# Kernel tuning notes

Hardware: AMD Instinct MI355X
Metric: run time of the kernel (lower is better)

The kernel has to match this reference:

```python
import jax, jax.numpy as jnp
import numpy as np

EPS = 1e-5
N_HEADS = 8
CLAMP = 100.0


def layernorm(x, g, b):
    m = x.mean(-1, keepdims=True)
    v = x.var(-1, keepdims=True)  # biased var, matches torch LayerNorm
    return (x - m) / jnp.sqrt(v + EPS) * g + b


def depthwise7(x, w, b):
    # x: [B,C,H,W], w: [C,1,7,7] depthwise (groups=C), pad=3
    y = jax.lax.conv_general_dilated(
        x, w, window_strides=(1, 1), padding=[(3, 3), (3, 3)],
        dimension_numbers=('NCHW', 'OIHW', 'NCHW'),
        feature_group_count=x.shape[1])
    return y + b[None, :, None, None]


def setup_inputs() -> dict:
    key = jax.random.key(0)
    ks = jax.random.split(key, 12)
    B, N, C = 8, 4096, 512
    KH = 7
    s = 0.02
    return {
        'x': jax.random.normal(ks[0], (B, N, C), jnp.float32),
        'qkv_w': jax.random.normal(ks[1], (C, 3 * C), jnp.float32) * s,
        'qkv_b': jnp.zeros((3 * C,), jnp.float32),
        'out_w': jax.random.normal(ks[2], (C, C), jnp.float32) * s,
        'out_b': jnp.zeros((C,), jnp.float32),
        'pre_g': jnp.ones((C,), jnp.float32),
        'pre_b': jnp.zeros((C,), jnp.float32),
        'lcm_g': jnp.ones((C,), jnp.float32),
        'lcm_b': jnp.zeros((C,), jnp.float32),
        'ci_w': jax.random.normal(ks[3], (C, 1, KH, KH), jnp.float32) * s,
        'ci_b': jnp.zeros((C,), jnp.float32),
        'bn_g': jnp.ones((C,), jnp.float32),
        'bn_b': jnp.zeros((C,), jnp.float32),
        'co_w': jax.random.normal(ks[4], (C, 1, KH, KH), jnp.float32) * s,
        'co_b': jnp.zeros((C,), jnp.float32),
        'H': 64,
        'W': 64,
    }


def reference(x, qkv_w, qkv_b, out_w, out_b, pre_g, pre_b, lcm_g, lcm_b,
              ci_w, ci_b, bn_g, bn_b, co_w, co_b, H, W):
    B, N, C = x.shape
    hd = C // N_HEADS
    normed = layernorm(x, pre_g, pre_b)
    qkv = normed @ qkv_w + qkv_b                       # [B,N,3C]
    qkv = qkv.reshape(B, N, 3, N_HEADS, hd).transpose(2, 0, 3, 1, 4)
    q = jax.nn.relu(qkv[0])                            # [B,h,N,d]
    k = jax.nn.relu(qkv[1])
    v = qkv[2]
    kv = jnp.einsum('bhnd,bhnv->bhdv', k, v)           # O(N d^2) associativity trick
    normalizer = jnp.maximum(k.sum(2, keepdims=True), CLAMP)  # [B,h,1,d]
    attn = jnp.einsum('bhnd,bhdv->bhnv', q, kv)
    denom = jnp.maximum((q * normalizer).sum(-1, keepdims=True), CLAMP)
    attn = attn / denom
    attn = attn.transpose(0, 2, 1, 3).reshape(B, N, C)
    attn = attn @ out_w + out_b
    # Local Concentration Module on lcm_norm(attn)
    t = layernorm(attn, lcm_g, lcm_b)
    xi = t.transpose(0, 2, 1).reshape(B, C, H, W)
    y = depthwise7(xi, ci_w, ci_b)
    y = jax.nn.gelu(y, approximate=False)
    m = y.mean((0, 2, 3), keepdims=True)               # BatchNorm2d training-mode stats
    var = y.var((0, 2, 3), keepdims=True)
    y = (y - m) / jnp.sqrt(var + EPS) * bn_g[None, :, None, None] + bn_b[None, :, None, None]
    y = depthwise7(y, co_w, co_b)
    lcm_out = y.reshape(B, C, N).transpose(0, 2, 1)
    return x + attn + lcm_out
```

## Files before the change

### kernel.cpp

```cpp
#include <hip/hip_runtime.h>
#include <math.h>

typedef short v8s __attribute__((ext_vector_type(8)));
typedef short v4s __attribute__((ext_vector_type(4)));
typedef float v4f __attribute__((ext_vector_type(4)));

__device__ __forceinline__ float b2f(unsigned short u) {
    return __uint_as_float(((unsigned)u) << 16);
}
__device__ __forceinline__ unsigned short f2b(float f) {
    unsigned u = __float_as_uint(f);
    unsigned r = (u + 0x7FFF + ((u >> 16) & 1)) >> 16;
    return (unsigned short)r;
}
__device__ __forceinline__ int swz8(int row) { return (row & 7) ^ ((row >> 3) & 7); }

__device__ __forceinline__ void gl_lds16(const unsigned short* g, unsigned short* l) {
    __builtin_amdgcn_global_load_lds(
        (const __attribute__((address_space(1))) void*)g,
        (__attribute__((address_space(3))) void*)l,
        16, 0, 0);
}

__global__ __launch_bounds__(256) void zero_fill(float* __restrict__ p, int n) {
    int i = blockIdx.x * 256 + threadIdx.x;
    if (i < n) p[i] = 0.0f;
}

__global__ __launch_bounds__(256) void ln_apply(const float* __restrict__ x,
                                                const float* __restrict__ g,
                                                const float* __restrict__ bt,
                                                unsigned short* __restrict__ out) {
    int t = threadIdx.x;
    int lane = t & 63, wave = t >> 6;
    size_t row = (size_t)blockIdx.x * 4 + wave;
    const float* p = x + row * 512 + lane * 8;
    float4 va = *(const float4*)p;
    float4 vb = *(const float4*)(p + 4);
    float s = va.x + va.y + va.z + va.w + vb.x + vb.y + vb.z + vb.w;
    float s2 = va.x * va.x + va.y * va.y + va.z * va.z + va.w * va.w +
               vb.x * vb.x + vb.y * vb.y + vb.z * vb.z + vb.w * vb.w;
    for (int o = 32; o > 0; o >>= 1) {
        s += __shfl_xor(s, o);
        s2 += __shfl_xor(s2, o);
    }
    float mean = s * (1.0f / 512.0f);
    float var = s2 * (1.0f / 512.0f) - mean * mean;
    float inv = rsqrtf(var + 1e-5f);
    float4 g0 = *(const float4*)(g + lane * 8);
    float4 g1 = *(const float4*)(g + lane * 8 + 4);
    float4 b0 = *(const float4*)(bt + lane * 8);
    float4 b1 = *(const float4*)(bt + lane * 8 + 4);
    v8s o8;
    o8[0] = (short)f2b((va.x - mean) * inv * g0.x + b0.x);
    o8[1] = (short)f2b((va.y - mean) * inv * g0.y + b0.y);
    o8[2] = (short)f2b((va.z - mean) * inv * g0.z + b0.z);
    o8[3] = (short)f2b((va.w - mean) * inv * g0.w + b0.w);
    o8[4] = (short)f2b((vb.x - mean) * inv * g1.x + b1.x);
    o8[5] = (short)f2b((vb.y - mean) * inv * g1.y + b1.y);
    o8[6] = (short)f2b((vb.z - mean) * inv * g1.z + b1.z);
    o8[7] = (short)f2b((vb.w - mean) * inv * g1.w + b1.w);
    *(v8s*)&out[row * 512 + lane * 8] = o8;
}

__global__ __launch_bounds__(256) void transpose_f2b(const float* __restrict__ in,
                                                     unsigned short* __restrict__ out,
                                                     int R, int C) {
    __shared__ unsigned short tile[32][33];
    int c0 = blockIdx.x * 32, r0 = blockIdx.y * 32;
    int tx = threadIdx.x, ty = threadIdx.y;
    for (int j = 0; j < 32; j += 8)
        tile[ty + j][tx] = f2b(in[(size_t)(r0 + ty + j) * C + c0 + tx]);
    __syncthreads();
    for (int j = 0; j < 32; j += 8)
        out[(size_t)(c0 + ty + j) * R + r0 + tx] = tile[tx][ty + j];
}

template <int NB, bool QKV>
__global__ __launch_bounds__(512, 4) void gemm256(const unsigned short* __restrict__ A,
                                                  const unsigned short* __restrict__ Bt,
                                                  const float* __restrict__ bias,
                                                  unsigned short* __restrict__ o0,
                                                  unsigned short* __restrict__ o1,
                                                  unsigned short* __restrict__ o2) {
    __shared__ __align__(16) unsigned short LB[3][12288];
    int t = threadIdx.x;
    int wave = t >> 6, lane = t & 63;
    int wm = wave >> 1, wn = wave & 1;
    int mrow = lane & 15, kq4 = lane >> 4;
    int nwg = gridDim.x;
    int cpx = nwg >> 3;
    int bid = blockIdx.x;
    int swz = (bid & 7) * cpx + (bid >> 3);
    int n0 = (swz % NB) * 128;
    int m0 = (swz / NB) * 256;
    const unsigned short* Ab = A + (size_t)m0 * 512;
    const unsigned short* Bb = Bt + (size_t)n0 * 512;
    int rA0 = t >> 2;
    int cA0 = (((t & 3) ^ ((rA0 >> 1) & 3)) * 8);
    int rA1 = 128 + (t >> 2);
    int cA1 = (((t & 3) ^ ((rA1 >> 1) & 3)) * 8);
    size_t srcA0 = (size_t)rA0 * 512 + cA0;
    size_t srcA1 = (size_t)rA1 * 512 + cA1;
    unsigned offA0 = wave * 512;
    unsigned offA1 = 4096 + wave * 512;
    unsigned offB  = 8192 + wave * 512;
    v4f acc[4][4] = {};
    int swr = ((kq4 ^ ((mrow >> 1) & 3)) * 8);

#define STAGE(kt, slot)                                          \
    do {                                                         \
        const unsigned short* aS = Ab + (size_t)(kt) * 32;       \
        const unsigned short* bS = Bb + (size_t)(kt) * 32;       \
        gl_lds16(aS + srcA0, &LB[slot][offA0]);                  \
        gl_lds16(aS + srcA1, &LB[slot][offA1]);                  \
        gl_lds16(bS + srcA0, &LB[slot][offB]);                   \
    } while (0)

    STAGE(0, 0);
    STAGE(1, 1);
    asm volatile("s_waitcnt vmcnt(3)" ::: "memory");
    __builtin_amdgcn_s_barrier();
    asm volatile("" ::: "memory");
    v8s cA[4], cB[4];
    {
        const unsigned short* as = LB[0];
        const unsigned short* bs = as + 8192;
#pragma unroll
        for (int i = 0; i < 4; i++) {
            cA[i] = *(const v8s*)&as[(wm * 64 + i * 16 + mrow) * 32 + swr];
            cB[i] = *(const v8s*)&bs[(wn * 64 + i * 16 + mrow) * 32 + swr];
        }
    }
#pragma unroll
    for (int kt = 0; kt < 16; ++kt) {
        __builtin_amdgcn_s_barrier();
        asm volatile("" ::: "memory");
        if (kt + 2 < 16) STAGE(kt + 2, (kt + 2) % 3);
        __builtin_amdgcn_s_setprio(1);
#pragma unroll
        for (int i = 0; i < 2; i++)
#pragma unroll
            for (int j = 0; j < 4; j++)
                acc[i][j] = __builtin_amdgcn_mfma_f32_16x16x32_bf16(cA[i], cB[j], acc[i][j], 0, 0, 0);
        v8s nA[4], nB[4];
        if (kt < 15) {
            if (kt < 14) {
                asm volatile("s_waitcnt vmcnt(3)" ::: "memory");
            } else {
                asm volatile("s_waitcnt vmcnt(0)" ::: "memory");
            }
            __builtin_amdgcn_s_barrier();
            asm volatile("" ::: "memory");
            const unsigned short* as = LB[(kt + 1) % 3];
            const unsigned short* bs = as + 8192;
#pragma unroll
            for (int i = 0; i < 4; i++) {
                nA[i] = *(const v8s*)&as[(wm * 64 + i * 16 + mrow) * 32 + swr];
                nB[i] = *(const v8s*)&bs[(wn * 64 + i * 16 + mrow) * 32 + swr];
            }
        }
#pragma unroll
        for (int i = 2; i < 4; i++)
#pragma unroll
            for (int j = 0; j < 4; j++)
                acc[i][j] = __builtin_amdgcn_mfma_f32_16x16x32_bf16(cA[i], cB[j], acc[i][j], 0, 0, 0);
        __builtin_amdgcn_s_setprio(0);
        if (kt < 15) {
#pragma unroll
            for (int i = 0; i < 4; i++) { cA[i] = nA[i]; cB[i] = nB[i]; }
        }
    }
#undef STAGE
    __syncthreads();
    unsigned short* CT = &LB[0][0];
    bool doRelu = QKV && (n0 < 1024);
#pragma unroll
    for (int j = 0; j < 4; j++) {
        int col = wn * 64 + j * 16 + mrow;
        float bv = bias[n0 + col];
        int gr = col >> 3, gb = col & 7;
#pragma unroll
        for (int i = 0; i < 4; i++) {
            int rowb = wm * 64 + i * 16 + kq4 * 4;
#pragma unroll
            for (int r = 0; r < 4; r++) {
                int row = rowb + r;
                float v = acc[i][j][r] + bv;
                if (doRelu) v = fmaxf(v, 0.0f);
                CT[row * 136 + ((gr ^ swz8(row)) << 3) + gb] = f2b(v);
            }
        }
    }
    __syncthreads();
    if (!QKV || n0 < 512) {
#pragma unroll
        for (int p = 0; p < 8; p++) {
            int g = p * 512 + t;
            int row = g >> 4, gl = g & 15;
            v8s v = *(const v8s*)&CT[row * 136 + ((gl ^ swz8(row)) << 3)];
            *(v8s*)&o0[(size_t)(m0 + row) * 512 + n0 + gl * 8] = v;
        }
    } else {
        unsigned short* Tb = (n0 < 1024) ? o1 : o2;
        int col = t >> 2, sub = t & 3;
        int cglob = n0 + col;
        int hl = (cglob & 511) >> 6, d = cglob & 63;
        int bb = m0 >> 12, gc = m0 & 4095;
        unsigned short* dst = Tb + ((size_t)((bb * 8 + hl) * 64 + d)) * 4096 + gc;
        int cg = col >> 3, cb7 = col & 7;
#pragma unroll
        for (int g = 0; g < 8; g++) {
            v8s v;
#pragma unroll
            for (int e = 0; e < 8; e++) {
                int rr = g * 32 + sub * 8 + e;
                v[e] = (short)CT[rr * 136 + ((cg ^ swz8(rr)) << 3) + cb7];
            }
            *(v8s*)&dst[g * 32 + sub * 8] = v;
        }
    }
}

__global__ __launch_bounds__(256) void kv_part(const unsigned short* __restrict__ kT,
                                               const unsigned short* __restrict__ vT,
                                               float* __restrict__ kvp,
                                               float* __restrict__ ksp) {
    __shared__ __align__(16) unsigned short LB[3][4096];
    int bh = blockIdx.x, nc = blockIdx.y;
    int t = threadIdx.x;
    int w = t >> 6, lane = t & 63;
    int wdk = w >> 1, wdv = w & 1;
    int mrow = lane & 15, kq4 = lane >> 4;
    const unsigned short* Kb = kT + (size_t)bh * 262144 + nc * 512;
    const unsigned short* Vb = vT + (size_t)bh * 262144 + nc * 512;
    int rA = t >> 2;
    int lcA = (t & 3) ^ (rA & 3);
    size_t srcoff = (size_t)rA * 4096 + lcA * 8;
    unsigned dstK = w * 512;
    unsigned dstV = 2048 + w * 512;
    v4f acc[2][2] = {};
    v4f accs[2] = {};
    v8s ones;
#pragma unroll
    for (int jj = 0; jj < 8; jj++) ones[jj] = (short)0x3F80;

#define KSTAGE(ks, slot)                                         \
    do {                                                         \
        gl_lds16(Kb + (size_t)(ks) * 32 + srcoff, &LB[slot][dstK]); \
        gl_lds16(Vb + (size_t)(ks) * 32 + srcoff, &LB[slot][dstV]); \
    } while (0)

    KSTAGE(0, 0);
    KSTAGE(1, 1);
    for (int ks = 0; ks < 16; ++ks) {
        if (ks < 15) {
            asm volatile("s_waitcnt vmcnt(2)" ::: "memory");
        } else {
            asm volatile("s_waitcnt vmcnt(0)" ::: "memory");
        }
        __builtin_amdgcn_s_barrier();
        asm volatile("" ::: "memory");
        if (ks + 2 < 16) KSTAGE(ks + 2, (ks + 2) % 3);
        const unsigned short* as = LB[ks % 3];
        v8s af[2], bf[2];
#pragma unroll
        for (int i = 0; i < 2; i++) {
            int row = wdk * 32 + i * 16 + mrow;
            af[i] = *(const v8s*)&as[row * 32 + ((kq4 ^ (row & 3)) << 3)];
        }
#pragma unroll
        for (int j = 0; j < 2; j++) {
            int row = wdv * 32 + j * 16 + mrow;
            bf[j] = *(const v8s*)&as[2048 + row * 32 + ((kq4 ^ (row & 3)) << 3)];
        }
#pragma unroll
        for (int i = 0; i < 2; i++)
#pragma unroll
            for (int j = 0; j < 2; j++)
                acc[i][j] = __builtin_amdgcn_mfma_f32_16x16x32_bf16(af[i], bf[j], acc[i][j], 0, 0, 0);
        if (wdv == 0) {
#pragma unroll
            for (int i = 0; i < 2; i++)
                accs[i] = __builtin_amdgcn_mfma_f32_16x16x32_bf16(af[i], ones, accs[i], 0, 0, 0);
        }
    }
#undef KSTAGE
    float* dst = kvp + ((size_t)(bh * 8 + nc)) * 4096;
#pragma unroll
    for (int i = 0; i < 2; i++)
#pragma unroll
        for (int j = 0; j < 2; j++)
#pragma unroll
            for (int r = 0; r < 4; r++) {
                int row = wdk * 32 + i * 16 + kq4 * 4 + r;
                int col = wdv * 32 + j * 16 + mrow;
                dst[row * 64 + col] = acc[i][j][r];
            }
    if (wdv == 0 && mrow == 0) {
        float* kd = ksp + ((size_t)(bh * 8 + nc)) * 64 + wdk * 32;
#pragma unroll
        for (int i = 0; i < 2; i++)
#pragma unroll
            for (int r = 0; r < 4; r++)
                kd[i * 16 + kq4 * 4 + r] = accs[i][r];
    }
}

__global__ __launch_bounds__(256) void kv_reduce(const float* __restrict__ kvp,
                                                 const float* __restrict__ ksp,
                                                 unsigned short* __restrict__ kvhT,
                                                 unsigned short* __restrict__ kvlT,
                                                 unsigned short* __restrict__ nrmp) {
    int tid = blockIdx.x * 256 + threadIdx.x;
    int bh = tid >> 12, e = tid & 4095;
    int dk = e >> 6, dv = e & 63;
    float s = 0.0f;
#pragma unroll
    for (int c = 0; c < 8; c++) s += kvp[((size_t)(bh * 8 + c)) * 4096 + e];
    unsigned short hb = f2b(s);
    kvhT[(size_t)bh * 4096 + dv * 64 + dk] = hb;
    kvlT[(size_t)bh * 4096 + dv * 64 + dk] = f2b(s - b2f(hb));
    if (tid < 4096) {
        int bh2 = tid >> 6, dk2 = tid & 63;
        float x = 0.0f;
#pragma unroll
        for (int c = 0; c < 8; c++) x += ksp[(bh2 * 8 + c) * 64 + dk2];
        x = fmaxf(x, 100.0f);
        unsigned short nh = f2b(x);
        nrmp[bh2 * 128 + dk2] = nh;
        nrmp[bh2 * 128 + 64 + dk2] = f2b(x - b2f(nh));
    }
}

__global__ __launch_bounds__(256) void attn_mfma(unsigned short* __restrict__ qa,
                                                 const unsigned short* __restrict__ kvhT,
                                                 const unsigned short* __restrict__ kvlT,
                                                 const unsigned short* __restrict__ nrmp) {
    __shared__ __align__(16) unsigned short olds[4][4096];
    int bh = blockIdx.y;
    int b = bh >> 3, h = bh & 7;
    int t = threadIdx.x;
    int w = t >> 6, lane = t & 63;
    int mrow = lane & 15, kq4 = lane >> 4;
    int nb = blockIdx.x * 256 + w * 64;
    unsigned short* qbase = qa + ((size_t)(b * 4096 + nb)) * 512 + h * 64;
    v4f acc[4][4] = {};
    v4f accd[4] = {};
#pragma unroll
    for (int s = 0; s < 2; s++) {
        v8s af[4];
#pragma unroll
        for (int i = 0; i < 4; i++)
            af[i] = *(const v8s*)&qbase[(size_t)(i * 16 + mrow) * 512 + s * 32 + kq4 * 8];
        v8s nh = *(const v8s*)&nrmp[bh * 128 + s * 32 + kq4 * 8];
        v8s nl = *(const v8s*)&nrmp[bh * 128 + 64 + s * 32 + kq4 * 8];
#pragma unroll
        for (int i = 0; i < 4; i++) {
            accd[i] = __builtin_amdgcn_mfma_f32_16x16x32_bf16(af[i], nh, accd[i], 0, 0, 0);
            accd[i] = __builtin_amdgcn_mfma_f32_16x16x32_bf16(af[i], nl, accd[i], 0, 0, 0);
        }
#pragma unroll
        for (int j = 0; j < 4; j++) {
            v8s kh = *(const v8s*)&kvhT[(size_t)bh * 4096 + (j * 16 + mrow) * 64 + s * 32 + kq4 * 8];
            v8s kl = *(const v8s*)&kvlT[(size_t)bh * 4096 + (j * 16 + mrow) * 64 + s * 32 + kq4 * 8];
#pragma unroll
            for (int i = 0; i < 4; i++) {
                acc[i][j] = __builtin_amdgcn_mfma_f32_16x16x32_bf16(af[i], kh, acc[i][j], 0, 0, 0);
                acc[i][j] = __builtin_amdgcn_mfma_f32_16x16x32_bf16(af[i], kl, acc[i][j], 0, 0, 0);
            }
        }
    }
    unsigned short* ol = olds[w];
#pragma unroll
    for (int i = 0; i < 4; i++) {
        float inv[4];
#pragma unroll
        for (int r = 0; r < 4; r++) inv[r] = 1.0f / fmaxf(accd[i][r], 100.0f);
#pragma unroll
        for (int j = 0; j < 4; j++) {
            int dv = j * 16 + mrow;
#pragma unroll
            for (int r = 0; r < 4; r++) {
                int rl = i * 16 + kq4 * 4 + r;
                ol[rl * 64 + (((dv >> 3) ^ (rl & 7)) << 3) + (dv & 7)] = f2b(acc[i][j][r] * inv[r]);
            }
        }
    }
    __syncthreads();
#pragma unroll
    for (int p = 0; p < 8; p++) {
        int idx = p * 64 + lane;
        int row = idx >> 3, gl = idx & 7;
        v8s v = *(const v8s*)&ol[row * 64 + ((gl ^ (row & 7)) << 3)];
        *(v8s*)&qbase[(size_t)row * 512 + gl * 8] = v;
    }
}

__global__ __launch_bounds__(256) void ln2_transpose(const unsigned short* __restrict__ in,
                                                     const float* __restrict__ g,
                                                     const float* __restrict__ bt,
                                                     unsigned short* __restrict__ out) {
    int bid = blockIdx.x;
    int b = bid >> 6;
    int n0 = (bid & 63) * 64;
    __shared__ float gs[512], bs[512];
    __shared__ __align__(16) unsigned short tile[512 * 64];
    int t = threadIdx.x;
    for (int i = t; i < 512; i += 256) { gs[i] = g[i]; bs[i] = bt[i]; }
    int nl = t >> 2, sub = t & 3;
    const unsigned short* src = in + ((size_t)(b * 4096 + n0 + nl)) * 512 + sub * 8;
    v8s vv[16];
#pragma unroll
    for (int c16 = 0; c16 < 16; c16++)
        vv[c16] = *(const v8s*)&src[c16 * 32];
    float s = 0.f, s2 = 0.f;
#pragma unroll
    for (int c16 = 0; c16 < 16; c16++)
#pragma unroll
        for (int j = 0; j < 8; j++) {
            float f = b2f((unsigned short)vv[c16][j]);
            s += f; s2 += f * f;
        }
    s += __shfl_xor(s, 1); s2 += __shfl_xor(s2, 1);
    s += __shfl_xor(s, 2); s2 += __shfl_xor(s2, 2);
    float mean = s * (1.f / 512.f);
    float var = s2 * (1.f / 512.f) - mean * mean;
    float inv = rsqrtf(var + 1e-5f);
    __syncthreads();
#pragma unroll
    for (int c16 = 0; c16 < 16; c16++) {
        int cb_ = sub * 8 + c16 * 32;
#pragma unroll
        for (int j = 0; j < 8; j++) {
            int c = cb_ + j;
            float f = b2f((unsigned short)vv[c16][j]);
            float y = (f - mean) * inv * gs[c] + bs[c];
            tile[c * 64 + ((((nl >> 3) ^ (c & 7)) << 3) | (nl & 7))] = f2b(y);
        }
    }
    __syncthreads();
    unsigned short* dst = out + ((size_t)b * 512) * 4096 + n0;
#pragma unroll
    for (int p = 0; p < 16; p++) {
        int chunk = p * 256 + t;
        int c = chunk >> 3, gseg = chunk & 7;
        int phys = gseg ^ (c & 7);
        v8s v = *(const v8s*)&tile[c * 64 + phys * 8];
        *(v8s*)&dst[(size_t)c * 4096 + gseg * 8] = v;
    }
}

__global__ __launch_bounds__(256) void dwconv7_gelu(const unsigned short* __restrict__ in,
                                                    const float* __restrict__ w,
                                                    const float* __restrict__ bias,
                                                    unsigned short* __restrict__ out,
                                                    float* __restrict__ bn_sum,
                                                    float* __restrict__ bn_sumsq) {
    int bc = blockIdx.x;
    int c = bc & 511;
    __shared__ float img[70 * 72];
    __shared__ float wsm[49];
    __shared__ float r1[4], r2[4];
    int t = threadIdx.x;
    int tx = t & 63, ty = t >> 6;
    for (int i = t; i < 70 * 72; i += 256) img[i] = 0.0f;
    if (t < 49) wsm[t] = w[c * 49 + t];
    __syncthreads();
    const unsigned short* src = in + (size_t)bc * 4096;
#pragma unroll
    for (int q = t; q < 512; q += 256) {
        v8s v = *(const v8s*)&src[q * 8];
        float* ip = &img[((q >> 3) + 3) * 72 + (q & 7) * 8 + 3];
#pragma unroll
        for (int j = 0; j < 8; j++) ip[j] = b2f((unsigned short)v[j]);
    }
    __syncthreads();
    float wt[49];
#pragma unroll
    for (int i = 0; i < 49; i++) wt[i] = wsm[i];
    float bv = bias[c];
    float acc[16];
#pragma unroll
    for (int i = 0; i < 16; i++) acc[i] = bv;
    int h0 = ty * 16;
#pragma unroll
    for (int rr = 0; rr < 22; rr++) {
        float v[7];
#pragma unroll
        for (int kw = 0; kw < 7; kw++) v[kw] = img[(h0 + rr) * 72 + tx + kw];
#pragma unroll
        for (int kh = 0; kh < 7; kh++) {
            int o = rr - kh;
            if (o >= 0 && o <= 15) {
                float dot = v[0] * wt[kh * 7];
#pragma unroll
                for (int kw = 1; kw < 7; kw++) dot += v[kw] * wt[kh * 7 + kw];
                acc[o] += dot;
            }
        }
    }
    float s = 0.0f, s2 = 0.0f;
    unsigned short* dst = out + (size_t)bc * 4096;
#pragma unroll
    for (int i = 0; i < 16; i++) {
        float a = acc[i];
        float ge = 0.5f * a * (1.0f + erff(a * 0.70710678118f));
        dst[(h0 + i) * 64 + tx] = f2b(ge);
        s += ge;
        s2 += ge * ge;
    }
    for (int o = 32; o > 0; o >>= 1) {
        s += __shfl_down(s, o);
        s2 += __shfl_down(s2, o);
    }
    int lane = t & 63;
    if (lane == 0) { r1[ty] = s; r2[ty] = s2; }
    __syncthreads();
    if (t == 0) {
        atomicAdd(&bn_sum[c], r1[0] + r1[1] + r1[2] + r1[3]);
        atomicAdd(&bn_sumsq[c], r2[0] + r2[1] + r2[2] + r2[3]);
    }
}

__global__ void bn_finalize(const float* __restrict__ s, const float* __restrict__ s2,
                            const float* __restrict__ g, const float* __restrict__ b,
                            float2* __restrict__ ab) {
    int c = blockIdx.x * blockDim.x + threadIdx.x;
    if (c >= 512) return;
    float m = s[c] * (1.0f / 32768.0f);
    float var = s2[c] * (1.0f / 32768.0f) - m * m;
    float inv = rsqrtf(var + 1e-5f);
    float sc = g[c] * inv;
    ab[c] = make_float2(sc, b[c] - m * sc);
}

__global__ __launch_bounds__(256) void dwconv7_bn(const unsigned short* __restrict__ in,
                                                  const float2* __restrict__ bnab,
                                                  const float* __restrict__ w,
                                                  const float* __restrict__ bias,
                                                  unsigned short* __restrict__ out) {
    int bc = blockIdx.x;
    int c = bc & 511;
    __shared__ float img[70 * 72];
    __shared__ float wsm[49];
    int t = threadIdx.x;
    int tx = t & 63, ty = t >> 6;
    for (int i = t; i < 70 * 72; i += 256) img[i] = 0.0f;
    if (t < 49) wsm[t] = w[c * 49 + t];
    __syncthreads();
    float2 ab = bnab[c];
    const unsigned short* src = in + (size_t)bc * 4096;
#pragma unroll
    for (int q = t; q < 512; q += 256) {
        v8s v = *(const v8s*)&src[q * 8];
        float* ip = &img[((q >> 3) + 3) * 72 + (q & 7) * 8 + 3];
#pragma unroll
        for (int j = 0; j < 8; j++) ip[j] = b2f((unsigned short)v[j]) * ab.x + ab.y;
    }
    __syncthreads();
    float wt[49];
#pragma unroll
    for (int i = 0; i < 49; i++) wt[i] = wsm[i];
    float bv = bias[c];
    float acc[16];
#pragma unroll
    for (int i = 0; i < 16; i++) acc[i] = bv;
    int h0 = ty * 16;
#pragma unroll
    for (int rr = 0; rr < 22; rr++) {
        float v[7];
#pragma unroll
        for (int kw = 0; kw < 7; kw++) v[kw] = img[(h0 + rr) * 72 + tx + kw];
#pragma unroll
        for (int kh = 0; kh < 7; kh++) {
            int o = rr - kh;
            if (o >= 0 && o <= 15) {
                float dot = v[0] * wt[kh * 7];
#pragma unroll
                for (int kw = 1; kw < 7; kw++) dot += v[kw] * wt[kh * 7 + kw];
                acc[o] += dot;
            }
        }
    }
    unsigned short* dst = out + (size_t)bc * 4096;
#pragma unroll
    for (int i = 0; i < 16; i++)
        dst[(h0 + i) * 64 + tx] = f2b(acc[i]);
}

__global__ __launch_bounds__(256) void final_add(const float* __restrict__ x,
                                                 const unsigned short* __restrict__ attn,
                                                 const unsigned short* __restrict__ y2,
                                                 float* __restrict__ out) {
    __shared__ unsigned short tile[32][36];
    int b = blockIdx.z;
    int c0 = blockIdx.x * 32;
    int n0b = blockIdx.y * 128;
    int t = threadIdx.x;
#pragma unroll
    for (int nt = 0; nt < 4; ++nt) {
        int n0 = n0b + nt * 32;
        __syncthreads();
        {
            int c = t >> 3, n4 = (t & 7) * 4;
            ushort4 v = *(const ushort4*)&y2[((size_t)(b * 512 + c0 + c)) * 4096 + n0 + n4];
            tile[c][n4] = v.x; tile[c][n4 + 1] = v.y; tile[c][n4 + 2] = v.z; tile[c][n4 + 3] = v.w;
        }
        __syncthreads();
        int nl = t >> 3, cl = (t & 7) * 4;
        size_t idx = ((size_t)(b * 4096 + n0 + nl)) * 512 + c0 + cl;
        float4 xv = *(const float4*)&x[idx];
        ushort4 av = *(const ushort4*)&attn[idx];
        float4 o;
        o.x = xv.x + b2f(av.x) + b2f(tile[cl][nl]);
        o.y = xv.y + b2f(av.y) + b2f(tile[cl + 1][nl]);
        o.z = xv.z + b2f(av.z) + b2f(tile[cl + 2][nl]);
        o.w = xv.w + b2f(av.w) + b2f(tile[cl + 3][nl]);
        *(float4*)&out[idx] = o;
    }
}

extern "C" void kernel_launch(void* const* d_in, const int* in_sizes, int n_in,
                              void* d_out, int out_size, void* d_ws, size_t ws_size,
                              hipStream_t stream) {
    const float* x     = (const float*)d_in[0];
    const float* qkv_w = (const float*)d_in[1];
    const float* qkv_b = (const float*)d_in[2];
    const float* out_w = (const float*)d_in[3];
    const float* out_b = (const float*)d_in[4];
    const float* pre_g = (const float*)d_in[5];
    const float* pre_b = (const float*)d_in[6];
    const float* lcm_g = (const float*)d_in[7];
    const float* lcm_b = (const float*)d_in[8];
    const float* ci_w  = (const float*)d_in[9];
    const float* ci_b  = (const float*)d_in[10];
    const float* bn_g  = (const float*)d_in[11];
    const float* bn_b  = (const float*)d_in[12];
    const float* co_w  = (const float*)d_in[13];
    const float* co_b  = (const float*)d_in[14];

    char* ws = (char*)d_ws;
    const size_t SLOT = 33554432;
    unsigned short* S0 = (unsigned short*)(ws);
    unsigned short* S1 = (unsigned short*)(ws + SLOT);
    unsigned short* S2 = (unsigned short*)(ws + 2 * SLOT);
    const size_t MISC = 3 * SLOT;
    unsigned short* wT1 = (unsigned short*)(ws + MISC);
    unsigned short* wT2 = (unsigned short*)(ws + MISC + 1572864);
    float* bn_sum       = (float*)(ws + MISC + 2097152);
    float* bn_sumsq     = (float*)(ws + MISC + 2097152 + 2048);
    float2* bnab        = (float2*)(ws + MISC + 2097152 + 4096);
    float* ksp          = (float*)(ws + MISC + 2105344);
    float* outp         = (float*)d_out;

    unsigned short* normed = (unsigned short*)d_out;
    float* kvp             = (float*)((char*)d_out + SLOT);
    unsigned short* kvhT   = (unsigned short*)((char*)d_out + SLOT + 8388608);
    unsigned short* kvlT   = kvhT + 262144;
    unsigned short* nrmp   = kvlT + 262144;

    dim3 tb(32, 8);
    transpose_f2b<<<dim3(48, 16), tb, 0, stream>>>(qkv_w, wT1, 512, 1536);
    transpose_f2b<<<dim3(16, 16), tb, 0, stream>>>(out_w, wT2, 512, 512);
    zero_fill<<<4, 256, 0, stream>>>(bn_sum, 1024);
    ln_apply<<<8192, 256, 0, stream>>>(x, pre_g, pre_b, normed);
    gemm256<12, true><<<1536, 512, 0, stream>>>(normed, wT1, qkv_b, S0, S1, S2);
    kv_part<<<dim3(64, 8), 256, 0, stream>>>(S1, S2, kvp, ksp);
    kv_reduce<<<1024, 256, 0, stream>>>(kvp, ksp, kvhT, kvlT, nrmp);
    attn_mfma<<<dim3(16, 64), 256, 0, stream>>>(S0, kvhT, kvlT, nrmp);
    gemm256<4, false><<<512, 512, 0, stream>>>(S0, wT2, out_b, S1, S1, S1);
    ln2_transpose<<<512, 256, 0, stream>>>(S1, lcm_g, lcm_b, S0);
    dwconv7_gelu<<<4096, 256, 0, stream>>>(S0, ci_w, ci_b, S2, bn_sum, bn_sumsq);
    bn_finalize<<<2, 256, 0, stream>>>(bn_sum, bn_sumsq, bn_g, bn_b, bnab);
    dwconv7_bn<<<4096, 256, 0, stream>>>(S2, bnab, co_w, co_b, S0);
    final_add<<<dim3(16, 32, 8), 256, 0, stream>>>(x, S1, S0, outp);
}
```

Measured before the change: 419.9 us.

## Use 256x256 QKV GEMM tile with deeper pipeline and merge prep kernels

Replaces the QKV projection GEMM with a new 256x256-tile kernel that uses 8 waves in a 2x4 layout, 128 KB of LDS and a four-slot, three-ahead global-to-LDS prefetch. The larger tile increases operand reuse and halves the workgroup count. It also rewrites the transposed K/V store to write contiguous 8-row chunks. The output-projection GEMM drops its register double-buffering in favour of a simpler load-then-MFMA loop, and the two weight transposes plus the zero fill are merged into one launch. The large LDS footprint and 128 accumulator registers per thread limit occupancy to one block per CU.

```diff
diff --git a/kernel.cpp b/kernel.cpp
--- a/kernel.cpp
+++ b/kernel.cpp
@@ -22,9 +22,36 @@
         16, 0, 0);
 }
 
-__global__ __launch_bounds__(256) void zero_fill(float* __restrict__ p, int n) {
-    int i = blockIdx.x * 256 + threadIdx.x;
-    if (i < n) p[i] = 0.0f;
+__global__ __launch_bounds__(256) void prep(const float* __restrict__ qkv_w,
+                                            const float* __restrict__ out_w,
+                                            unsigned short* __restrict__ wT1,
+                                            unsigned short* __restrict__ wT2,
+                                            float* __restrict__ zf) {
+    __shared__ unsigned short tile[32][33];
+    int bid = blockIdx.x;
+    int t = threadIdx.x;
+    if (bid >= 1024) {
+        int i = (bid - 1024) * 256 + t;
+        if (i < 1024) zf[i] = 0.0f;
+        return;
+    }
+    const float* in;
+    unsigned short* out;
+    int R, C, c0, r0;
+    if (bid < 768) {
+        in = qkv_w; out = wT1; R = 512; C = 1536;
+        c0 = (bid % 48) * 32; r0 = (bid / 48) * 32;
+    } else {
+        in = out_w; out = wT2; R = 512; C = 512;
+        int b2 = bid - 768;
+        c0 = (b2 % 16) * 32; r0 = (b2 / 16) * 32;
+    }
+    int tx = t & 31, ty = t >> 5;
+    for (int j = 0; j < 32; j += 8)
+        tile[ty + j][tx] = f2b(in[(size_t)(r0 + ty + j) * C + c0 + tx]);
+    __syncthreads();
+    for (int j = 0; j < 32; j += 8)
+        out[(size_t)(c0 + ty + j) * R + r0 + tx] = tile[tx][ty + j];
 }
 
 __global__ __launch_bounds__(256) void ln_apply(const float* __restrict__ x,
@@ -63,37 +90,140 @@
     *(v8s*)&out[row * 512 + lane * 8] = o8;
 }
 
-__global__ __launch_bounds__(256) void transpose_f2b(const float* __restrict__ in,
-                                                     unsigned short* __restrict__ out,
-                                                     int R, int C) {
-    __shared__ unsigned short tile[32][33];
-    int c0 = blockIdx.x * 32, r0 = blockIdx.y * 32;
-    int tx = threadIdx.x, ty = threadIdx.y;
-    for (int j = 0; j < 32; j += 8)
-        tile[ty + j][tx] = f2b(in[(size_t)(r0 + ty + j) * C + c0 + tx]);
-    __syncthreads();
-    for (int j = 0; j < 32; j += 8)
-        out[(size_t)(c0 + ty + j) * R + r0 + tx] = tile[tx][ty + j];
-}
-
-template <int NB, bool QKV>
-__global__ __launch_bounds__(512, 4) void gemm256(const unsigned short* __restrict__ A,
-                                                  const unsigned short* __restrict__ Bt,
-                                                  const float* __restrict__ bias,
-                                                  unsigned short* __restrict__ o0,
-                                                  unsigned short* __restrict__ o1,
-                                                  unsigned short* __restrict__ o2) {
+__global__ __launch_bounds__(512) void gemm8p(const unsigned short* __restrict__ A,
+                                              const unsigned short* __restrict__ Bt,
+                                              const float* __restrict__ bias,
+                                              unsigned short* __restrict__ o0,
+                                              unsigned short* __restrict__ o1,
+                                              unsigned short* __restrict__ o2) {
+    __shared__ __align__(16) unsigned short LB[65536];
+    int t = threadIdx.x;
+    int wave = t >> 6, lane = t & 63;
+    int wm = wave >> 2, wn = wave & 3;
+    int mrow = lane & 15, kq4 = lane >> 4;
+    int cpx = gridDim.x >> 3;
+    int bid = blockIdx.x;
+    int swz = (bid & 7) * cpx + (bid >> 3);
+    int n0 = (swz % 6) * 256;
+    int m0 = (swz / 6) * 256;
+    const unsigned short* Ab = A + (size_t)m0 * 512;
+    const unsigned short* Bb = Bt + (size_t)n0 * 512;
+    int rr0 = t >> 2;
+    int cs = ((t & 3) ^ (rr0 & 3)) * 8;
+    size_t rowoff0 = (size_t)rr0 * 512 + cs;
+    size_t rowoff1 = rowoff0 + (size_t)128 * 512;
+    unsigned woff = wave * 512;
+    v4f acc[8][4] = {};
+    int swr = ((kq4 ^ (mrow & 3)) << 3);
+
+#define STAGE_CP(g)                                                        \
+    do {                                                                   \
+        const unsigned short* As_ = Ab + ((g) >> 1) * 64 + ((g) & 1) * 32; \
+        const unsigned short* Bs_ = Bb + ((g) >> 1) * 64 + ((g) & 1) * 32; \
+        unsigned rg = ((((g) >> 1) & 1) << 15) + (((g) & 1) << 13);        \
+        gl_lds16(As_ + rowoff0, &LB[rg + woff]);                           \
+        gl_lds16(As_ + rowoff1, &LB[rg + 4096 + woff]);                    \
+        gl_lds16(Bs_ + rowoff0, &LB[rg + 16384 + woff]);                   \
+        gl_lds16(Bs_ + rowoff1, &LB[rg + 16384 + 4096 + woff]);            \
+    } while (0)
+
+    STAGE_CP(0);
+    STAGE_CP(1);
+    STAGE_CP(2);
+#pragma unroll
+    for (int G = 0; G < 16; ++G) {
+        if (G <= 13) {
+            asm volatile("s_waitcnt vmcnt(8)" ::: "memory");
+        } else if (G == 14) {
+            asm volatile("s_waitcnt vmcnt(4)" ::: "memory");
+        } else {
+            asm volatile("s_waitcnt vmcnt(0)" ::: "memory");
+        }
+        __builtin_amdgcn_s_barrier();
+        asm volatile("" ::: "memory");
+        if (G + 3 < 16) STAGE_CP(G + 3);
+        unsigned base = (((G >> 1) & 1) << 15) + ((G & 1) << 13);
+        const unsigned short* as = &LB[base];
+        const unsigned short* bs = &LB[base + 16384];
+        v8s af[8], bf[4];
+#pragma unroll
+        for (int i = 0; i < 8; i++)
+            af[i] = *(const v8s*)&as[(wm * 128 + i * 16 + mrow) * 32 + swr];
+#pragma unroll
+        for (int j = 0; j < 4; j++)
+            bf[j] = *(const v8s*)&bs[(wn * 64 + j * 16 + mrow) * 32 + swr];
+        __builtin_amdgcn_s_setprio(1);
+#pragma unroll
+        for (int i = 0; i < 8; i++)
+#pragma unroll
+            for (int j = 0; j < 4; j++)
+                acc[i][j] = __builtin_amdgcn_mfma_f32_16x16x32_bf16(af[i], bf[j], acc[i][j], 0, 0, 0);
+        __builtin_amdgcn_s_setprio(0);
+    }
+#undef STAGE_CP
+    __syncthreads();
+    bool doRelu = (n0 < 1024);
+#pragma unroll
+    for (int j = 0; j < 4; j++) {
+        int col = wn * 64 + j * 16 + mrow;
+        float bv = bias[n0 + col];
+        int gr = col >> 3, gb = col & 7;
+#pragma unroll
+        for (int i = 0; i < 8; i++) {
+            int rowb = wm * 128 + i * 16 + kq4 * 4;
+#pragma unroll
+            for (int r = 0; r < 4; r++) {
+                int row = rowb + r;
+                float v = acc[i][j][r] + bv;
+                if (doRelu) v = fmaxf(v, 0.0f);
+                LB[row * 256 + ((gr ^ swz8(row)) << 3) + gb] = f2b(v);
+            }
+        }
+    }
+    __syncthreads();
+    if (n0 < 512) {
+#pragma unroll
+        for (int p = 0; p < 16; p++) {
+            int g = p * 512 + t;
+            int row = g >> 5, gl = g & 31;
+            v8s v = *(const v8s*)&LB[row * 256 + ((gl ^ swz8(row)) << 3)];
+            *(v8s*)&o0[(size_t)(m0 + row) * 512 + n0 + gl * 8] = v;
+        }
+    } else {
+        unsigned short* Tb = (n0 < 1024) ? o1 : o2;
+        int bb = m0 >> 12, gc = m0 & 4095;
+#pragma unroll
+        for (int p = 0; p < 16; p++) {
+            int chunk = p * 512 + t;
+            int c = chunk >> 5, rseg = chunk & 31;
+            int cglob = n0 + c;
+            int hl = (cglob & 511) >> 6, d = cglob & 63;
+            int cg = c >> 3, cb7 = c & 7;
+            v8s v;
+#pragma unroll
+            for (int e = 0; e < 8; e++) {
+                int rowi = rseg * 8 + e;
+                v[e] = (short)LB[rowi * 256 + ((cg ^ swz8(rowi)) << 3) + cb7];
+            }
+            *(v8s*)&Tb[((size_t)((bb * 8 + hl) * 64 + d)) * 4096 + gc + rseg * 8] = v;
+        }
+    }
+}
+
+__global__ __launch_bounds__(512, 4) void gemm2k(const unsigned short* __restrict__ A,
+                                                 const unsigned short* __restrict__ Bt,
+                                                 const float* __restrict__ bias,
+                                                 unsigned short* __restrict__ o0) {
     __shared__ __align__(16) unsigned short LB[3][12288];
     int t = threadIdx.x;
     int wave = t >> 6, lane = t & 63;
     int wm = wave >> 1, wn = wave & 1;
     int mrow = lane & 15, kq4 = lane >> 4;
-    int nwg = gridDim.x;
-    int cpx = nwg >> 3;
+    int cpx = gridDim.x >> 3;
     int bid = blockIdx.x;
     int swz = (bid & 7) * cpx + (bid >> 3);
-    int n0 = (swz % NB) * 128;
-    int m0 = (swz / NB) * 256;
+    int n0 = (swz % 4) * 128;
+    int m0 = (swz / 4) * 256;
     const unsigned short* Ab = A + (size_t)m0 * 512;
     const unsigned short* Bb = Bt + (size_t)n0 * 512;
     int rA0 = t >> 2;
@@ -119,62 +249,35 @@
 
     STAGE(0, 0);
     STAGE(1, 1);
-    asm volatile("s_waitcnt vmcnt(3)" ::: "memory");
-    __builtin_amdgcn_s_barrier();
-    asm volatile("" ::: "memory");
-    v8s cA[4], cB[4];
-    {
-        const unsigned short* as = LB[0];
-        const unsigned short* bs = as + 8192;
-#pragma unroll
-        for (int i = 0; i < 4; i++) {
-            cA[i] = *(const v8s*)&as[(wm * 64 + i * 16 + mrow) * 32 + swr];
-            cB[i] = *(const v8s*)&bs[(wn * 64 + i * 16 + mrow) * 32 + swr];
-        }
-    }
-#pragma unroll
     for (int kt = 0; kt < 16; ++kt) {
+        if (kt < 15) {
+            asm volatile("s_waitcnt vmcnt(3)" ::: "memory");
+        } else {
+            asm volatile("s_waitcnt vmcnt(0)" ::: "memory");
+        }
         __builtin_amdgcn_s_barrier();
         asm volatile("" ::: "memory");
         if (kt + 2 < 16) STAGE(kt + 2, (kt + 2) % 3);
+        const unsigned short* as = LB[kt % 3];
+        const unsigned short* bs = LB[kt % 3] + 8192;
+        v8s af[4], bf[4];
+#pragma unroll
+        for (int i = 0; i < 4; i++)
+            af[i] = *(const v8s*)&as[(wm * 64 + i * 16 + mrow) * 32 + swr];
+#pragma unroll
+        for (int j = 0; j < 4; j++)
+            bf[j] = *(const v8s*)&bs[(wn * 64 + j * 16 + mrow) * 32 + swr];
         __builtin_amdgcn_s_setprio(1);
 #pragma unroll
-        for (int i = 0; i < 2; i++)
+        for (int i = 0; i < 4; i++)
 #pragma unroll
             for (int j = 0; j < 4; j++)
-                acc[i][j] = __builtin_amdgcn_mfma_f32_16x16x32_bf16(cA[i], cB[j], acc[i][j], 0, 0, 0);
-        v8s nA[4], nB[4];
-        if (kt < 15) {
-            if (kt < 14) {
-                asm volatile("s_waitcnt vmcnt(3)" ::: "memory");
-            } else {
-                asm volatile("s_waitcnt vmcnt(0)" ::: "memory");
-            }
-            __builtin_amdgcn_s_barrier();
-            asm volatile("" ::: "memory");
-            const unsigned short* as = LB[(kt + 1) % 3];
-            const unsigned short* bs = as + 8192;
-#pragma unroll
-            for (int i = 0; i < 4; i++) {
-                nA[i] = *(const v8s*)&as[(wm * 64 + i * 16 + mrow) * 32 + swr];
-                nB[i] = *(const v8s*)&bs[(wn * 64 + i * 16 + mrow) * 32 + swr];
-            }
-        }
-#pragma unroll
-        for (int i = 2; i < 4; i++)
-#pragma unroll
-            for (int j = 0; j < 4; j++)
-                acc[i][j] = __builtin_amdgcn_mfma_f32_16x16x32_bf16(cA[i], cB[j], acc[i][j], 0, 0, 0);
+                acc[i][j] = __builtin_amdgcn_mfma_f32_16x16x32_bf16(af[i], bf[j], acc[i][j], 0, 0, 0);
         __builtin_amdgcn_s_setprio(0);
-        if (kt < 15) {
-#pragma unroll
-            for (int i = 0; i < 4; i++) { cA[i] = nA[i]; cB[i] = nB[i]; }
-        }
     }
 #undef STAGE
     __syncthreads();
     unsigned short* CT = &LB[0][0];
-    bool doRelu = QKV && (n0 < 1024);
 #pragma unroll
     for (int j = 0; j < 4; j++) {
         int col = wn * 64 + j * 16 + mrow;
@@ -186,39 +289,17 @@
 #pragma unroll
             for (int r = 0; r < 4; r++) {
                 int row = rowb + r;
-                float v = acc[i][j][r] + bv;
-                if (doRelu) v = fmaxf(v, 0.0f);
-                CT[row * 136 + ((gr ^ swz8(row)) << 3) + gb] = f2b(v);
+                CT[row * 136 + ((gr ^ swz8(row)) << 3) + gb] = f2b(acc[i][j][r] + bv);
             }
         }
     }
     __syncthreads();
-    if (!QKV || n0 < 512) {
-#pragma unroll
-        for (int p = 0; p < 8; p++) {
-            int g = p * 512 + t;
-            int row = g >> 4, gl = g & 15;
-            v8s v = *(const v8s*)&CT[row * 136 + ((gl ^ swz8(row)) << 3)];
-            *(v8s*)&o0[(size_t)(m0 + row) * 512 + n0 + gl * 8] = v;
-        }
-    } else {
-        unsigned short* Tb = (n0 < 1024) ? o1 : o2;
-        int col = t >> 2, sub = t & 3;
-        int cglob = n0 + col;
-        int hl = (cglob & 511) >> 6, d = cglob & 63;
-        int bb = m0 >> 12, gc = m0 & 4095;
-        unsigned short* dst = Tb + ((size_t)((bb * 8 + hl) * 64 + d)) * 4096 + gc;
-        int cg = col >> 3, cb7 = col & 7;
-#pragma unroll
-        for (int g = 0; g < 8; g++) {
-            v8s v;
-#pragma unroll
-            for (int e = 0; e < 8; e++) {
-                int rr = g * 32 + sub * 8 + e;
-                v[e] = (short)CT[rr * 136 + ((cg ^ swz8(rr)) << 3) + cb7];
-            }
-            *(v8s*)&dst[g * 32 + sub * 8] = v;
-        }
+#pragma unroll
+    for (int p = 0; p < 8; p++) {
+        int g = p * 512 + t;
+        int row = g >> 4, gl = g & 15;
+        v8s v = *(const v8s*)&CT[row * 136 + ((gl ^ swz8(row)) << 3)];
+        *(v8s*)&o0[(size_t)(m0 + row) * 512 + n0 + gl * 8] = v;
     }
 }
 
@@ -245,8 +326,8 @@
 #pragma unroll
     for (int jj = 0; jj < 8; jj++) ones[jj] = (short)0x3F80;
 
-#define KSTAGE(ks, slot)                                         \
-    do {                                                         \
+#define KSTAGE(ks, slot)                                            \
+    do {                                                            \
         gl_lds16(Kb + (size_t)(ks) * 32 + srcoff, &LB[slot][dstK]); \
         gl_lds16(Vb + (size_t)(ks) * 32 + srcoff, &LB[slot][dstV]); \
     } while (0)
@@ -660,16 +741,13 @@
     unsigned short* kvlT   = kvhT + 262144;
     unsigned short* nrmp   = kvlT + 262144;
 
-    dim3 tb(32, 8);
-    transpose_f2b<<<dim3(48, 16), tb, 0, stream>>>(qkv_w, wT1, 512, 1536);
-    transpose_f2b<<<dim3(16, 16), tb, 0, stream>>>(out_w, wT2, 512, 512);
-    zero_fill<<<4, 256, 0, stream>>>(bn_sum, 1024);
+    prep<<<1028, 256, 0, stream>>>(qkv_w, out_w, wT1, wT2, bn_sum);
     ln_apply<<<8192, 256, 0, stream>>>(x, pre_g, pre_b, normed);
-    gemm256<12, true><<<1536, 512, 0, stream>>>(normed, wT1, qkv_b, S0, S1, S2);
+    gemm8p<<<768, 512, 0, stream>>>(normed, wT1, qkv_b, S0, S1, S2);
     kv_part<<<dim3(64, 8), 256, 0, stream>>>(S1, S2, kvp, ksp);
     kv_reduce<<<1024, 256, 0, stream>>>(kvp, ksp, kvhT, kvlT, nrmp);
     attn_mfma<<<dim3(16, 64), 256, 0, stream>>>(S0, kvhT, kvlT, nrmp);
-    gemm256<4, false><<<512, 512, 0, stream>>>(S0, wT2, out_b, S1, S1, S1);
+    gemm2k<<<512, 512, 0, stream>>>(S0, wT2, out_b, S1);
     ln2_transpose<<<512, 256, 0, stream>>>(S1, lcm_g, lcm_b, S0);
     dwconv7_gelu<<<4096, 256, 0, stream>>>(S0, ci_w, ci_b, S2, bn_sum, bn_sumsq);
     bn_finalize<<<2, 256, 0, stream>>>(bn_sum, bn_sumsq, bn_g, bn_b, bnab);
```

Result: slower. 440.7 us (+5.0%).

## Merge prep kernels, fold BN finalize into conv, simplify GEMM main loop

Applied to the files above, without the earlier changes.

Merges the weight transposes, the zero fill and the first layernorm into one launch (prep_ln). Folds the batch-norm finalize step into dwconv7_bn, which now computes its per-channel scale and shift in-block. Together these remove four kernel launches and their serialization gaps. The GEMM main loop drops its software-pipelined register double-buffering of LDS fragments in favour of a simpler wait, barrier, load, then MFMA sequence, which may expose LDS latency but cuts register pressure.

```diff
diff --git a/kernel.cpp b/kernel.cpp
--- a/kernel.cpp
+++ b/kernel.cpp
@@ -22,58 +22,73 @@
         16, 0, 0);
 }
 
-__global__ __launch_bounds__(256) void zero_fill(float* __restrict__ p, int n) {
-    int i = blockIdx.x * 256 + threadIdx.x;
-    if (i < n) p[i] = 0.0f;
-}
-
-__global__ __launch_bounds__(256) void ln_apply(const float* __restrict__ x,
-                                                const float* __restrict__ g,
-                                                const float* __restrict__ bt,
-                                                unsigned short* __restrict__ out) {
-    int t = threadIdx.x;
-    int lane = t & 63, wave = t >> 6;
-    size_t row = (size_t)blockIdx.x * 4 + wave;
-    const float* p = x + row * 512 + lane * 8;
-    float4 va = *(const float4*)p;
-    float4 vb = *(const float4*)(p + 4);
-    float s = va.x + va.y + va.z + va.w + vb.x + vb.y + vb.z + vb.w;
-    float s2 = va.x * va.x + va.y * va.y + va.z * va.z + va.w * va.w +
-               vb.x * vb.x + vb.y * vb.y + vb.z * vb.z + vb.w * vb.w;
-    for (int o = 32; o > 0; o >>= 1) {
-        s += __shfl_xor(s, o);
-        s2 += __shfl_xor(s2, o);
-    }
-    float mean = s * (1.0f / 512.0f);
-    float var = s2 * (1.0f / 512.0f) - mean * mean;
-    float inv = rsqrtf(var + 1e-5f);
-    float4 g0 = *(const float4*)(g + lane * 8);
-    float4 g1 = *(const float4*)(g + lane * 8 + 4);
-    float4 b0 = *(const float4*)(bt + lane * 8);
-    float4 b1 = *(const float4*)(bt + lane * 8 + 4);
-    v8s o8;
-    o8[0] = (short)f2b((va.x - mean) * inv * g0.x + b0.x);
-    o8[1] = (short)f2b((va.y - mean) * inv * g0.y + b0.y);
-    o8[2] = (short)f2b((va.z - mean) * inv * g0.z + b0.z);
-    o8[3] = (short)f2b((va.w - mean) * inv * g0.w + b0.w);
-    o8[4] = (short)f2b((vb.x - mean) * inv * g1.x + b1.x);
-    o8[5] = (short)f2b((vb.y - mean) * inv * g1.y + b1.y);
-    o8[6] = (short)f2b((vb.z - mean) * inv * g1.z + b1.z);
-    o8[7] = (short)f2b((vb.w - mean) * inv * g1.w + b1.w);
-    *(v8s*)&out[row * 512 + lane * 8] = o8;
-}
-
-__global__ __launch_bounds__(256) void transpose_f2b(const float* __restrict__ in,
-                                                     unsigned short* __restrict__ out,
-                                                     int R, int C) {
+__global__ __launch_bounds__(256) void prep_ln(const float* __restrict__ x,
+                                               const float* __restrict__ pre_g,
+                                               const float* __restrict__ pre_b,
+                                               unsigned short* __restrict__ normed,
+                                               const float* __restrict__ qkv_w,
+                                               const float* __restrict__ out_w,
+                                               unsigned short* __restrict__ wT1,
+                                               unsigned short* __restrict__ wT2,
+                                               float* __restrict__ zf) {
     __shared__ unsigned short tile[32][33];
-    int c0 = blockIdx.x * 32, r0 = blockIdx.y * 32;
-    int tx = threadIdx.x, ty = threadIdx.y;
+    int bid = blockIdx.x;
+    int t = threadIdx.x;
+    if (bid < 8192) {
+        int lane = t & 63, wave = t >> 6;
+        size_t row = (size_t)bid * 4 + wave;
+        const float* p = x + row * 512 + lane * 8;
+        float4 va = *(const float4*)p;
+        float4 vb = *(const float4*)(p + 4);
+        float s = va.x + va.y + va.z + va.w + vb.x + vb.y + vb.z + vb.w;
+        float s2 = va.x * va.x + va.y * va.y + va.z * va.z + va.w * va.w +
+                   vb.x * vb.x + vb.y * vb.y + vb.z * vb.z + vb.w * vb.w;
+        for (int o = 32; o > 0; o >>= 1) {
+            s += __shfl_xor(s, o);
+            s2 += __shfl_xor(s2, o);
+        }
+        float mean = s * (1.0f / 512.0f);
+        float var = s2 * (1.0f / 512.0f) - mean * mean;
+        float inv = rsqrtf(var + 1e-5f);
+        float4 g0 = *(const float4*)(pre_g + lane * 8);
+        float4 g1 = *(const float4*)(pre_g + lane * 8 + 4);
+        float4 b0 = *(const float4*)(pre_b + lane * 8);
+        float4 b1 = *(const float4*)(pre_b + lane * 8 + 4);
+        v8s o8;
+        o8[0] = (short)f2b((va.x - mean) * inv * g0.x + b0.x);
+        o8[1] = (short)f2b((va.y - mean) * inv * g0.y + b0.y);
+        o8[2] = (short)f2b((va.z - mean) * inv * g0.z + b0.z);
+        o8[3] = (short)f2b((va.w - mean) * inv * g0.w + b0.w);
+        o8[4] = (short)f2b((vb.x - mean) * inv * g1.x + b1.x);
+        o8[5] = (short)f2b((vb.y - mean) * inv * g1.y + b1.y);
+        o8[6] = (short)f2b((vb.z - mean) * inv * g1.z + b1.z);
+        o8[7] = (short)f2b((vb.w - mean) * inv * g1.w + b1.w);
+        *(v8s*)&normed[row * 512 + lane * 8] = o8;
+        return;
+    }
+    int b2_ = bid - 8192;
+    if (b2_ >= 1024) {
+        int i = (b2_ - 1024) * 256 + t;
+        if (i < 1024) zf[i] = 0.0f;
+        return;
+    }
+    const float* in;
+    unsigned short* out;
+    int C, c0, r0;
+    if (b2_ < 768) {
+        in = qkv_w; out = wT1; C = 1536;
+        c0 = (b2_ % 48) * 32; r0 = (b2_ / 48) * 32;
+    } else {
+        in = out_w; out = wT2; C = 512;
+        int b3 = b2_ - 768;
+        c0 = (b3 % 16) * 32; r0 = (b3 / 16) * 32;
+    }
+    int tx = t & 31, ty = t >> 5;
     for (int j = 0; j < 32; j += 8)
         tile[ty + j][tx] = f2b(in[(size_t)(r0 + ty + j) * C + c0 + tx]);
     __syncthreads();
     for (int j = 0; j < 32; j += 8)
-        out[(size_t)(c0 + ty + j) * R + r0 + tx] = tile[tx][ty + j];
+        out[(size_t)(c0 + ty + j) * 512 + r0 + tx] = tile[tx][ty + j];
 }
 
 template <int NB, bool QKV>
@@ -119,57 +134,31 @@
 
     STAGE(0, 0);
     STAGE(1, 1);
-    asm volatile("s_waitcnt vmcnt(3)" ::: "memory");
-    __builtin_amdgcn_s_barrier();
-    asm volatile("" ::: "memory");
-    v8s cA[4], cB[4];
-    {
-        const unsigned short* as = LB[0];
-        const unsigned short* bs = as + 8192;
-#pragma unroll
-        for (int i = 0; i < 4; i++) {
-            cA[i] = *(const v8s*)&as[(wm * 64 + i * 16 + mrow) * 32 + swr];
-            cB[i] = *(const v8s*)&bs[(wn * 64 + i * 16 + mrow) * 32 + swr];
-        }
-    }
-#pragma unroll
     for (int kt = 0; kt < 16; ++kt) {
+        if (kt < 15) {
+            asm volatile("s_waitcnt vmcnt(3)" ::: "memory");
+        } else {
+            asm volatile("s_waitcnt vmcnt(0)" ::: "memory");
+        }
         __builtin_amdgcn_s_barrier();
         asm volatile("" ::: "memory");
         if (kt + 2 < 16) STAGE(kt + 2, (kt + 2) % 3);
+        const unsigned short* as = LB[kt % 3];
+        const unsigned short* bs = LB[kt % 3] + 8192;
+        v8s af[4], bf[4];
+#pragma unroll
+        for (int i = 0; i < 4; i++)
+            af[i] = *(const v8s*)&as[(wm * 64 + i * 16 + mrow) * 32 + swr];
+#pragma unroll
+        for (int j = 0; j < 4; j++)
+            bf[j] = *(const v8s*)&bs[(wn * 64 + j * 16 + mrow) * 32 + swr];
         __builtin_amdgcn_s_setprio(1);
 #pragma unroll
-        for (int i = 0; i < 2; i++)
+        for (int i = 0; i < 4; i++)
 #pragma unroll
             for (int j = 0; j < 4; j++)
-                acc[i][j] = __builtin_amdgcn_mfma_f32_16x16x32_bf16(cA[i], cB[j], acc[i][j], 0, 0, 0);
-        v8s nA[4], nB[4];
-        if (kt < 15) {
-            if (kt < 14) {
-                asm volatile("s_waitcnt vmcnt(3)" ::: "memory");
-            } else {
-                asm volatile("s_waitcnt vmcnt(0)" ::: "memory");
-            }
-            __builtin_amdgcn_s_barrier();
-            asm volatile("" ::: "memory");
-            const unsigned short* as = LB[(kt + 1) % 3];
-            const unsigned short* bs = as + 8192;
-#pragma unroll
-            for (int i = 0; i < 4; i++) {
-                nA[i] = *(const v8s*)&as[(wm * 64 + i * 16 + mrow) * 32 + swr];
-                nB[i] = *(const v8s*)&bs[(wn * 64 + i * 16 + mrow) * 32 + swr];
-            }
-        }
-#pragma unroll
-        for (int i = 2; i < 4; i++)
-#pragma unroll
-            for (int j = 0; j < 4; j++)
-                acc[i][j] = __builtin_amdgcn_mfma_f32_16x16x32_bf16(cA[i], cB[j], acc[i][j], 0, 0, 0);
+                acc[i][j] = __builtin_amdgcn_mfma_f32_16x16x32_bf16(af[i], bf[j], acc[i][j], 0, 0, 0);
         __builtin_amdgcn_s_setprio(0);
-        if (kt < 15) {
-#pragma unroll
-            for (int i = 0; i < 4; i++) { cA[i] = nA[i]; cB[i] = nB[i]; }
-        }
     }
 #undef STAGE
     __syncthreads();
@@ -245,8 +234,8 @@
 #pragma unroll
     for (int jj = 0; jj < 8; jj++) ones[jj] = (short)0x3F80;
 
-#define KSTAGE(ks, slot)                                         \
-    do {                                                         \
+#define KSTAGE(ks, slot)                                            \
+    do {                                                            \
         gl_lds16(Kb + (size_t)(ks) * 32 + srcoff, &LB[slot][dstK]); \
         gl_lds16(Vb + (size_t)(ks) * 32 + srcoff, &LB[slot][dstV]); \
     } while (0)
@@ -523,20 +512,11 @@
     }
 }
 
-__global__ void bn_finalize(const float* __restrict__ s, const float* __restrict__ s2,
-                            const float* __restrict__ g, const float* __restrict__ b,
-                            float2* __restrict__ ab) {
-    int c = blockIdx.x * blockDim.x + threadIdx.x;
-    if (c >= 512) return;
-    float m = s[c] * (1.0f / 32768.0f);
-    float var = s2[c] * (1.0f / 32768.0f) - m * m;
-    float inv = rsqrtf(var + 1e-5f);
-    float sc = g[c] * inv;
-    ab[c] = make_float2(sc, b[c] - m * sc);
-}
-
 __global__ __launch_bounds__(256) void dwconv7_bn(const unsigned short* __restrict__ in,
-                                                  const float2* __restrict__ bnab,
+                                                  const float* __restrict__ bn_sum,
+                                                  const float* __restrict__ bn_sumsq,
+                                                  const float* __restrict__ bn_g,
+                                                  const float* __restrict__ bn_b,
                                                   const float* __restrict__ w,
                                                   const float* __restrict__ bias,
                                                   unsigned short* __restrict__ out) {
@@ -544,12 +524,20 @@
     int c = bc & 511;
     __shared__ float img[70 * 72];
     __shared__ float wsm[49];
+    __shared__ float2 absh;
     int t = threadIdx.x;
     int tx = t & 63, ty = t >> 6;
     for (int i = t; i < 70 * 72; i += 256) img[i] = 0.0f;
     if (t < 49) wsm[t] = w[c * 49 + t];
-    __syncthreads();
-    float2 ab = bnab[c];
+    if (t == 0) {
+        float m = bn_sum[c] * (1.0f / 32768.0f);
+        float var = bn_sumsq[c] * (1.0f / 32768.0f) - m * m;
+        float inv = rsqrtf(var + 1e-5f);
+        float sc = bn_g[c] * inv;
+        absh = make_float2(sc, bn_b[c] - m * sc);
+    }
+    __syncthreads();
+    float2 ab = absh;
     const unsigned short* src = in + (size_t)bc * 4096;
 #pragma unroll
     for (int q = t; q < 512; q += 256) {
@@ -650,7 +638,6 @@
     unsigned short* wT2 = (unsigned short*)(ws + MISC + 1572864);
     float* bn_sum       = (float*)(ws + MISC + 2097152);
     float* bn_sumsq     = (float*)(ws + MISC + 2097152 + 2048);
-    float2* bnab        = (float2*)(ws + MISC + 2097152 + 4096);
     float* ksp          = (float*)(ws + MISC + 2105344);
     float* outp         = (float*)d_out;
 
@@ -660,11 +647,7 @@
     unsigned short* kvlT   = kvhT + 262144;
     unsigned short* nrmp   = kvlT + 262144;
 
-    dim3 tb(32, 8);
-    transpose_f2b<<<dim3(48, 16), tb, 0, stream>>>(qkv_w, wT1, 512, 1536);
-    transpose_f2b<<<dim3(16, 16), tb, 0, stream>>>(out_w, wT2, 512, 512);
-    zero_fill<<<4, 256, 0, stream>>>(bn_sum, 1024);
-    ln_apply<<<8192, 256, 0, stream>>>(x, pre_g, pre_b, normed);
+    prep_ln<<<9220, 256, 0, stream>>>(x, pre_g, pre_b, normed, qkv_w, out_w, wT1, wT2, bn_sum);
     gemm256<12, true><<<1536, 512, 0, stream>>>(normed, wT1, qkv_b, S0, S1, S2);
     kv_part<<<dim3(64, 8), 256, 0, stream>>>(S1, S2, kvp, ksp);
     kv_reduce<<<1024, 256, 0, stream>>>(kvp, ksp, kvhT, kvlT, nrmp);
@@ -672,7 +655,6 @@
     gemm256<4, false><<<512, 512, 0, stream>>>(S0, wT2, out_b, S1, S1, S1);
     ln2_transpose<<<512, 256, 0, stream>>>(S1, lcm_g, lcm_b, S0);
     dwconv7_gelu<<<4096, 256, 0, stream>>>(S0, ci_w, ci_b, S2, bn_sum, bn_sumsq);
-    bn_finalize<<<2, 256, 0, stream>>>(bn_sum, bn_sumsq, bn_g, bn_b, bnab);
-    dwconv7_bn<<<4096, 256, 0, stream>>>(S2, bnab, co_w, co_b, S0);
+    dwconv7_bn<<<4096, 256, 0, stream>>>(S2, bn_sum, bn_sumsq, bn_g, bn_b, co_w, co_b, S0);
     final_add<<<dim3(16, 32, 8), 256, 0, stream>>>(x, S1, S0, outp);
 }
```

Result: slower. 442.1 us (+5.3%).
